# Optimization experiments

Hardware: AMD Instinct MI355X
Metric: run time of the kernel (lower is better)

Reference implementation:

```python
import jax, jax.numpy as jnp
import numpy as np

NUM_GRAPHS = 128


def _gcn_conv(x, W, b, src, dst, norm, n_nodes):
    # PyG GCNConv: linear transform, then symmetric-normalized scatter-add aggregation
    h = x @ W                                  # [N, out]
    msg = norm[:, None] * h[src]               # [E+N, out] gathered messages
    out = jax.ops.segment_sum(msg, dst, num_segments=n_nodes)
    return out + b


def setup_inputs() -> dict:
    key = jax.random.key(0)
    ks = jax.random.split(key, 12)
    N, E, H, GE, C = 100000, 1000000, 64, 64, 5
    x = jax.random.normal(ks[0], (N, 2), dtype=jnp.float32)
    edge_index = jax.random.randint(ks[1], (2, E), 0, N, dtype=jnp.int32)
    batch = jnp.sort(jax.random.randint(ks[2], (N,), 0, NUM_GRAPHS, dtype=jnp.int32))
    graph_embedding = jax.random.normal(ks[3], (NUM_GRAPHS, GE), dtype=jnp.float32)
    s = lambda k, shape, fan: jax.random.normal(k, shape, dtype=jnp.float32) * (1.0 / np.sqrt(fan))
    W1 = s(ks[4], (2, H), 2); b1 = jnp.zeros((H,), jnp.float32)
    W2 = s(ks[5], (H, H), H); b2 = jnp.zeros((H,), jnp.float32)
    W3 = s(ks[6], (H, H), H); b3 = jnp.zeros((H,), jnp.float32)
    Wl = s(ks[7], (H + GE, C), H + GE); bl = jnp.zeros((C,), jnp.float32)
    return {"x": x, "edge_index": edge_index, "batch": batch,
            "graph_embedding": graph_embedding,
            "W1": W1, "b1": b1, "W2": W2, "b2": b2, "W3": W3, "b3": b3,
            "Wl": Wl, "bl": bl}


def reference(x, edge_index, batch, graph_embedding, W1, b1, W2, b2, W3, b3, Wl, bl):
    N = x.shape[0]
    loops = jnp.arange(N, dtype=edge_index.dtype)
    src = jnp.concatenate([edge_index[0], loops])   # add self-loops
    dst = jnp.concatenate([edge_index[1], loops])
    deg = jax.ops.segment_sum(jnp.ones_like(dst, dtype=x.dtype), dst, num_segments=N)
    dinv = jnp.where(deg > 0, jax.lax.rsqrt(deg), 0.0)
    norm = dinv[src] * dinv[dst]                    # [E+N]

    h = jax.nn.relu(_gcn_conv(x, W1, b1, src, dst, norm, N))
    h = jax.nn.relu(_gcn_conv(h, W2, b2, src, dst, norm, N))
    h = _gcn_conv(h, W3, b3, src, dst, norm, N)

    # global mean pool over graphs
    sums = jax.ops.segment_sum(h, batch, num_segments=NUM_GRAPHS)
    cnts = jax.ops.segment_sum(jnp.ones((N,), x.dtype), batch, num_segments=NUM_GRAPHS)
    pooled = sums / jnp.maximum(cnts, 1.0)[:, None]

    z = jnp.concatenate([pooled, graph_embedding], axis=1) @ Wl + bl
    return jax.nn.log_softmax(z, axis=1)
```

## Files before the change

### kernel.cpp

```cpp
#include <hip/hip_runtime.h>
#include <hip/hip_bf16.h>
#include <math.h>

#define NG 128
#define CHUNKB 4096
#define NBIN 512
#define EWIN 256

typedef __attribute__((ext_vector_type(8))) short short8;
typedef __attribute__((ext_vector_type(4))) float float4v;

static __device__ __forceinline__ float bf2f(__hip_bfloat16 v) { return __bfloat162float(v); }

__global__ void k_bin_hist(const int* __restrict__ dst, int* __restrict__ hist,
                           int e, int nb) {
    __shared__ int h[NBIN];
    for (int i = threadIdx.x; i < NBIN; i += 256) h[i] = 0;
    __syncthreads();
    int base = blockIdx.x * CHUNKB;
    int lim = e - base; if (lim > CHUNKB) lim = CHUNKB;
    for (int k = threadIdx.x; k < lim; k += 256)
        atomicAdd(&h[dst[base + k] >> 8], 1);
    __syncthreads();
    for (int b = threadIdx.x; b < NBIN; b += 256) hist[b * nb + blockIdx.x] = h[b];
}

__global__ void __launch_bounds__(512) genscan1(int* __restrict__ a, int* __restrict__ bsums, int n) {
    __shared__ int s[512];
    int tid = threadIdx.x;
    int i = blockIdx.x * 512 + tid;
    int v = (i < n) ? a[i] : 0;
    s[tid] = v;
    __syncthreads();
    for (int d = 1; d < 512; d <<= 1) {
        int t = (tid >= d) ? s[tid - d] : 0;
        __syncthreads();
        s[tid] += t;
        __syncthreads();
    }
    if (i < n) a[i] = s[tid] - v;
    if (tid == 511) bsums[blockIdx.x] = s[511];
}

__global__ void __launch_bounds__(512) genscan2(int* __restrict__ bsums, int nb) {
    __shared__ int s[512];
    int tid = threadIdx.x;
    int v = (tid < nb) ? bsums[tid] : 0;
    s[tid] = v;
    __syncthreads();
    for (int d = 1; d < 512; d <<= 1) {
        int t = (tid >= d) ? s[tid - d] : 0;
        __syncthreads();
        s[tid] += t;
        __syncthreads();
    }
    if (tid < nb) bsums[tid] = s[tid] - v;
}

__global__ void k_bin_scatter(const int* __restrict__ srcs, const int* __restrict__ dsts,
                              const int* __restrict__ offsets, const int* __restrict__ bsums,
                              int2* __restrict__ outbuf, int e, int nb) {
    __shared__ int hcnt[NBIN];
    __shared__ int lstart[NBIN];
    __shared__ int ss[256];
    __shared__ int2 stage[CHUNKB];
    int tid = threadIdx.x, blk = blockIdx.x, base = blk * CHUNKB;
    int lim = e - base; if (lim > CHUNKB) lim = CHUNKB;
    for (int i = tid; i < NBIN; i += 256) hcnt[i] = 0;
    __syncthreads();
    for (int k = tid; k < lim; k += 256)
        atomicAdd(&hcnt[dsts[base + k] >> 8], 1);
    __syncthreads();
    int c0 = hcnt[2 * tid], c1 = hcnt[2 * tid + 1];
    int sum = c0 + c1;
    ss[tid] = sum;
    __syncthreads();
    for (int d = 1; d < 256; d <<= 1) {
        int t = (tid >= d) ? ss[tid - d] : 0;
        __syncthreads();
        ss[tid] += t;
        __syncthreads();
    }
    int excl = ss[tid] - sum;
    lstart[2 * tid] = excl;
    lstart[2 * tid + 1] = excl + c0;
    __syncthreads();
    hcnt[2 * tid] = excl;
    hcnt[2 * tid + 1] = excl + c0;
    __syncthreads();
    for (int k = tid; k < lim; k += 256) {
        int2 ed = make_int2(srcs[base + k], dsts[base + k]);
        int p = atomicAdd(&hcnt[ed.y >> 8], 1);
        stage[p] = ed;
    }
    __syncthreads();
    for (int i = tid; i < NBIN; i += 256) {
        int gi = i * nb + blk;
        lstart[i] = offsets[gi] + bsums[gi >> 9] - lstart[i];
    }
    __syncthreads();
    for (int p = tid; p < lim; p += 256) {
        int2 ed = stage[p];
        outbuf[lstart[ed.y >> 8] + p] = ed;
    }
}

__global__ void k_csrA(const int2* __restrict__ ebuck, const int* __restrict__ offsets,
                       const int* __restrict__ bsums, int* __restrict__ row_ptr,
                       float* __restrict__ dinv, int n, int nb, int nbuk, int e_total) {
    __shared__ int lcnt[256];
    __shared__ int ssc[256];
    int b = blockIdx.x, tid = threadIdx.x, n0 = b << 8;
    lcnt[tid] = 0;
    __syncthreads();
    int i0 = b * nb, i1 = (b + 1) * nb;
    int e0 = offsets[i0] + bsums[i0 >> 9];
    int e1 = offsets[i1] + bsums[i1 >> 9];
    for (int i = e0 + tid; i < e1; i += 256)
        atomicAdd(&lcnt[ebuck[i].y - n0], 1);
    __syncthreads();
    int v = lcnt[tid];
    ssc[tid] = v;
    __syncthreads();
    for (int d = 1; d < 256; d <<= 1) {
        int t = (tid >= d) ? ssc[tid - d] : 0;
        __syncthreads();
        ssc[tid] += t;
        __syncthreads();
    }
    int node = n0 + tid;
    if (node < n) {
        row_ptr[node] = e0 + ssc[tid] - v;
        dinv[node] = rsqrtf((float)v + 1.0f);
        if (node == n - 1) row_ptr[n] = e_total;
    }
}

__global__ void k_csrB(const int2* __restrict__ ebuck, const int* __restrict__ offsets,
                       const int* __restrict__ bsums, const int* __restrict__ row_ptr,
                       const float* __restrict__ dinv, int2* __restrict__ csr, int nb) {
    __shared__ int lcur[256];
    int b = blockIdx.x, tid = threadIdx.x, n0 = b << 8;
    lcur[tid] = 0;
    __syncthreads();
    int i0 = b * nb, i1 = (b + 1) * nb;
    int e0 = offsets[i0] + bsums[i0 >> 9];
    int e1 = offsets[i1] + bsums[i1 >> 9];
    for (int i = e0 + tid; i < e1; i += 256) {
        int2 ed = ebuck[i];
        int r = atomicAdd(&lcur[ed.y - n0], 1);
        int pos = row_ptr[ed.y] + r;
        float w = dinv[ed.x] * dinv[ed.y];
        csr[pos] = make_int2(ed.x, __float_as_int(w));
    }
}

__global__ void k_layer1(const int* __restrict__ row_ptr, const int2* __restrict__ edges,
                         const float* __restrict__ x, const float* __restrict__ dinv,
                         const float* __restrict__ W1, const float* __restrict__ b1,
                         __hip_bfloat16* __restrict__ h, int n) {
    __shared__ float w1s[128];
    __shared__ float b1s[64];
    if (threadIdx.x < 128) w1s[threadIdx.x] = W1[threadIdx.x];
    if (threadIdx.x < 64) b1s[threadIdx.x] = b1[threadIdx.x];
    __syncthreads();
    int i = blockIdx.x * blockDim.x + threadIdx.x;
    if (i >= n) return;
    const float2* x2 = (const float2*)x;
    float dd = dinv[i], d2 = dd * dd;
    float2 xi = x2[i];
    float a0 = d2 * xi.x, a1 = d2 * xi.y;
    int lo = row_ptr[i], hi = row_ptr[i + 1];
    int k = lo;
    for (; k + 4 <= hi; k += 4) {
        int2 e0 = edges[k], e1 = edges[k + 1], e2 = edges[k + 2], e3 = edges[k + 3];
        float2 v0 = x2[e0.x], v1 = x2[e1.x], v2 = x2[e2.x], v3 = x2[e3.x];
        a0 += __int_as_float(e0.y) * v0.x; a1 += __int_as_float(e0.y) * v0.y;
        a0 += __int_as_float(e1.y) * v1.x; a1 += __int_as_float(e1.y) * v1.y;
        a0 += __int_as_float(e2.y) * v2.x; a1 += __int_as_float(e2.y) * v2.y;
        a0 += __int_as_float(e3.y) * v3.x; a1 += __int_as_float(e3.y) * v3.y;
    }
    for (; k < hi; k++) {
        int2 e = edges[k];
        float2 v = x2[e.x];
        a0 += __int_as_float(e.y) * v.x;
        a1 += __int_as_float(e.y) * v.y;
    }
    short8* hv = reinterpret_cast<short8*>(h + (size_t)i * 64);
    #pragma unroll
    for (int g = 0; g < 8; g++) {
        short8 pack;
        #pragma unroll
        for (int j = 0; j < 8; j++) {
            int col = g * 8 + j;
            float v = fmaxf(a0 * w1s[col] + a1 * w1s[64 + col] + b1s[col], 0.0f);
            __hip_bfloat16 bv = __float2bfloat16(v);
            pack[j] = *reinterpret_cast<short*>(&bv);
        }
        hv[g] = pack;
    }
}

template <bool FAST>
static __device__ __forceinline__ void agg_node(int lo, int hi, int half, int col,
        const int2* __restrict__ gE, const int2* EW, int wave_lo,
        const uint* __restrict__ hinu, float& ax, float& ay) {
    for (int k = lo; k < hi; k += 16) {
        int ss[8]; float ww[8];
        #pragma unroll
        for (int j = 0; j < 8; j++) {
            int idx = k + 2 * j + half;
            int cidx = idx < hi ? idx : lo;
            int2 ee = FAST ? EW[cidx - wave_lo] : gE[cidx];
            ss[j] = ee.x;
            ww[j] = idx < hi ? __int_as_float(ee.y) : 0.0f;
        }
        uint vv[8];
        #pragma unroll
        for (int j = 0; j < 8; j++) vv[j] = hinu[(size_t)ss[j] * 32 + col];
        #pragma unroll
        for (int j = 0; j < 8; j++) {
            ax += ww[j] * __int_as_float(vv[j] << 16);
            ay += ww[j] * __int_as_float(vv[j] & 0xffff0000u);
        }
    }
}

template <int RELU, int POOL>
__global__ void __launch_bounds__(64, 8) k_aggLin(const int* __restrict__ row_ptr,
                                                  const int2* __restrict__ edges,
                                                  const __hip_bfloat16* __restrict__ hin,
                                                  const float* __restrict__ dinv,
                                                  const __hip_bfloat16* __restrict__ Wf,
                                                  const float* __restrict__ b,
                                                  __hip_bfloat16* __restrict__ hout,
                                                  const int* __restrict__ batch,
                                                  float* __restrict__ sums, int n) {
    __shared__ __attribute__((aligned(16))) __hip_bfloat16 T[16 * 72];
    __shared__ int2 EW[EWIN];
    int lane = threadIdx.x;
    int nb0 = blockIdx.x * 16;
    if (nb0 >= n) return;
    int half = lane >> 5, col = lane & 31;
    const uint* hinu = reinterpret_cast<const uint*>(hin);

    int bidx = nb0 + (lane < 16 ? lane : 16);
    if (bidx > n) bidx = n;
    int rp = row_ptr[bidx];
    int wave_lo = __shfl(rp, 0);
    int wave_hi = __shfl(rp, 16);
    int cnt = wave_hi - wave_lo;
    bool fast = (cnt <= EWIN);
    if (fast)
        for (int i = lane; i < cnt; i += 64) EW[i] = edges[wave_lo + i];

    for (int nn = 0; nn < 16; nn++) {
        int node = nb0 + nn;
        float ax = 0.0f, ay = 0.0f;
        if (node < n) {
            if (half == 0) {
                float dn = dinv[node];
                uint hv = hinu[(size_t)node * 32 + col];
                float dn2 = dn * dn;
                ax = dn2 * __int_as_float(hv << 16);
                ay = dn2 * __int_as_float(hv & 0xffff0000u);
            }
            int lo = __shfl(rp, nn), hi = __shfl(rp, nn + 1);
            if (fast) agg_node<true >(lo, hi, half, col, edges, EW, wave_lo, hinu, ax, ay);
            else      agg_node<false>(lo, hi, half, col, edges, EW, wave_lo, hinu, ax, ay);
        }
        ax += __shfl_xor(ax, 32);
        ay += __shfl_xor(ay, 32);
        if (half == 0) {
            __hip_bfloat16 bx = __float2bfloat16(ax);
            __hip_bfloat16 by = __float2bfloat16(ay);
            uint pack = (uint)(*reinterpret_cast<unsigned short*>(&bx)) |
                        ((uint)(*reinterpret_cast<unsigned short*>(&by)) << 16);
            *reinterpret_cast<uint*>(&T[nn * 72 + 2 * col]) = pack;
        }
    }

    int m = lane & 15, q = lane >> 4;
    short8 a0 = *reinterpret_cast<const short8*>(&T[m * 72 + q * 8]);
    short8 a1 = *reinterpret_cast<const short8*>(&T[m * 72 + 32 + q * 8]);
    int lastn = nb0 + 15 < n ? nb0 + 15 : n - 1;
    bool onegraph = POOL && (nb0 + 15 < n) && (batch[nb0] == batch[lastn]);
    int gA = POOL ? batch[nb0] : 0;
    #pragma unroll
    for (int jt = 0; jt < 4; jt++) {
        short8 bf0 = *reinterpret_cast<const short8*>(Wf + ((size_t)(jt * 2 + 0) * 64 + lane) * 8);
        short8 bf1 = *reinterpret_cast<const short8*>(Wf + ((size_t)(jt * 2 + 1) * 64 + lane) * 8);
        float4v d = {0.0f, 0.0f, 0.0f, 0.0f};
        d = __builtin_amdgcn_mfma_f32_16x16x32_bf16(a0, bf0, d, 0, 0, 0);
        d = __builtin_amdgcn_mfma_f32_16x16x32_bf16(a1, bf1, d, 0, 0, 0);
        float bias = b[jt * 16 + m];
        if (POOL) {
            if (onegraph) {
                float s = (d[0] + bias) + (d[1] + bias) + (d[2] + bias) + (d[3] + bias);
                s += __shfl_xor(s, 16);
                s += __shfl_xor(s, 32);
                if (q == 0) atomicAdd(&sums[gA * 64 + jt * 16 + m], s);
            } else {
                #pragma unroll
                for (int r = 0; r < 4; r++) {
                    int node = nb0 + q * 4 + r;
                    if (node < n)
                        atomicAdd(&sums[batch[node] * 64 + jt * 16 + m], d[r] + bias);
                }
            }
        } else {
            #pragma unroll
            for (int r = 0; r < 4; r++) {
                int node = nb0 + q * 4 + r;
                if (node < n) {
                    float v = d[r] + bias;
                    if (RELU) v = fmaxf(v, 0.0f);
                    hout[(size_t)node * 64 + jt * 16 + m] = __float2bfloat16(v);
                }
            }
        }
    }
}

__global__ void k_prepW(const float* __restrict__ W2, const float* __restrict__ W3,
                        __hip_bfloat16* __restrict__ Wf2, __hip_bfloat16* __restrict__ Wf3) {
    const float* W = blockIdx.x ? W3 : W2;
    __hip_bfloat16* Wf = blockIdx.x ? Wf3 : Wf2;
    int t = threadIdx.x;
    int c = t >> 6, l = t & 63;
    int jt = c >> 1, half = c & 1, nn = l & 15, q = l >> 4;
    #pragma unroll
    for (int j = 0; j < 8; j++) {
        int k = half * 32 + q * 8 + j;
        Wf[t * 8 + j] = __float2bfloat16(W[k * 64 + jt * 16 + nn]);
    }
}

__device__ inline int lower_bound_i(const int* __restrict__ a, int n, int key) {
    int lo = 0, hi = n;
    while (lo < hi) {
        int mid = (lo + hi) >> 1;
        if (a[mid] < key) lo = mid + 1; else hi = mid;
    }
    return lo;
}

__global__ void k_head(const float* __restrict__ sums, const int* __restrict__ batch,
                       const float* __restrict__ ge, const float* __restrict__ Wl,
                       const float* __restrict__ bl, float* __restrict__ out,
                       int n, int ng) {
    int g = blockIdx.x * blockDim.x + threadIdx.x;
    if (g < ng) {
        int lo = lower_bound_i(batch, n, g);
        int hi = lower_bound_i(batch, n, g + 1);
        float c = fmaxf((float)(hi - lo), 1.0f);
        float z[5];
        for (int cl = 0; cl < 5; cl++) z[cl] = bl[cl];
        for (int k = 0; k < 64; k++) {
            float p = sums[g * 64 + k] / c;
            for (int cl = 0; cl < 5; cl++) z[cl] += p * Wl[k * 5 + cl];
        }
        for (int k = 0; k < 64; k++) {
            float p = ge[g * 64 + k];
            for (int cl = 0; cl < 5; cl++) z[cl] += p * Wl[(64 + k) * 5 + cl];
        }
        float m = z[0];
        for (int cl = 1; cl < 5; cl++) m = fmaxf(m, z[cl]);
        float s = 0.0f;
        for (int cl = 0; cl < 5; cl++) s += expf(z[cl] - m);
        float lse = m + logf(s);
        for (int cl = 0; cl < 5; cl++) out[g * 5 + cl] = z[cl] - lse;
    }
}

#define ALIGN16(x) (((x) + 15) & ~(size_t)15)

extern "C" void kernel_launch(void* const* d_in, const int* in_sizes, int n_in,
                              void* d_out, int out_size, void* d_ws, size_t ws_size,
                              hipStream_t stream) {
    const float* x    = (const float*)d_in[0];
    const int*   ei   = (const int*)d_in[1];
    const int*   batch= (const int*)d_in[2];
    const float* ge   = (const float*)d_in[3];
    const float* W1   = (const float*)d_in[4];
    const float* b1   = (const float*)d_in[5];
    const float* W2   = (const float*)d_in[6];
    const float* b2   = (const float*)d_in[7];
    const float* W3   = (const float*)d_in[8];
    const float* b3   = (const float*)d_in[9];
    const float* Wl   = (const float*)d_in[10];
    const float* bl   = (const float*)d_in[11];
    float* out = (float*)d_out;

    const int N = in_sizes[0] / 2;
    const int E = in_sizes[1] / 2;
    const int* src = ei;
    const int* dst = ei + E;
    const int NBUK = (N + 255) >> 8;
    const int nbC  = (E + CHUNKB - 1) / CHUNKB;

    char* wsb = (char*)d_ws;
    float* dinv   = (float*)wsb;                wsb += ALIGN16((size_t)N * 4);
    __hip_bfloat16* h16 = (__hip_bfloat16*)wsb;  wsb += ALIGN16((size_t)64 * N * 2);
    __hip_bfloat16* buf2= (__hip_bfloat16*)wsb;  wsb += ALIGN16((size_t)64 * N * 2);
    float* sums   = (float*)wsb;                wsb += ALIGN16((size_t)NG * 64 * 4);
    __hip_bfloat16* Wf2 = (__hip_bfloat16*)wsb; wsb += ALIGN16((size_t)4096 * 2);
    __hip_bfloat16* Wf3 = (__hip_bfloat16*)wsb; wsb += ALIGN16((size_t)4096 * 2);
    int2*  ebuck  = (int2*)wsb;                 wsb += ALIGN16((size_t)E * 8);
    int2*  csr    = (int2*)wsb;                 wsb += ALIGN16((size_t)E * 8);
    int*   row_ptr= (int*)wsb;                  wsb += ALIGN16((size_t)(N + 1) * 4);
    int*   hist   = (int*)wsb;                  wsb += ALIGN16((size_t)NBIN * nbC * 4);
    int*   bsums  = (int*)wsb;                  wsb += 512 * 4;

    const int BS = 256;
    int gN   = (N + BS - 1) / BS;
    int gF   = (N + 15) / 16;
    int nH   = NBIN * nbC;
    int gH   = (nH + 511) / 512;

    hipMemsetAsync(sums, 0, (size_t)NG * 64 * 4, stream);
    k_bin_hist<<<nbC, BS, 0, stream>>>(dst, hist, E, nbC);
    genscan1<<<gH, 512, 0, stream>>>(hist, bsums, nH);
    genscan2<<<1, 512, 0, stream>>>(bsums, gH);
    k_bin_scatter<<<nbC, BS, 0, stream>>>(src, dst, hist, bsums, ebuck, E, nbC);
    k_csrA<<<NBUK, BS, 0, stream>>>(ebuck, hist, bsums, row_ptr, dinv, N, nbC, NBUK, E);
    k_csrB<<<NBUK, BS, 0, stream>>>(ebuck, hist, bsums, row_ptr, dinv, csr, nbC);
    k_prepW<<<2, 512, 0, stream>>>(W2, W3, Wf2, Wf3);

    k_layer1<<<gN, BS, 0, stream>>>(row_ptr, csr, x, dinv, W1, b1, h16, N);

    k_aggLin<1, 0><<<gF, 64, 0, stream>>>(row_ptr, csr, h16, dinv, Wf2, b2, buf2,
                                          nullptr, nullptr, N);

    k_aggLin<0, 1><<<gF, 64, 0, stream>>>(row_ptr, csr, buf2, dinv, Wf3, b3, nullptr,
                                          batch, sums, N);

    k_head<<<1, 128, 0, stream>>>(sums, batch, ge, Wl, bl, out, N, NG);
}
```

Measured before the change: 231.1 us.

## Fold symmetric normalization into node features and drop per-edge weights from CSR

Instead of storing a per-edge weight dinv[src]*dinv[dst], each layer's output is pre-scaled by dinv of the source node and the aggregate is post-scaled by dinv of the destination node. The CSR then holds only int source indices, which halves edge bandwidth in every aggregation pass and removes the multiplies. The two CSR-build kernels are merged into one that stages edges in LDS, and the memset and weight prep are folded into the histogram kernel as extra blocks, removing several launches. The LDS stage is large (about 48KB), which may reduce occupancy of the CSR kernel, and there is a global-memory fallback path for oversized buckets.

```diff
diff --git a/kernel.cpp b/kernel.cpp
--- a/kernel.cpp
+++ b/kernel.cpp
@@ -6,23 +6,44 @@
 #define CHUNKB 4096
 #define NBIN 512
 #define EWIN 256
+#define STAGE_CAP 6144
 
 typedef __attribute__((ext_vector_type(8))) short short8;
 typedef __attribute__((ext_vector_type(4))) float float4v;
 
-static __device__ __forceinline__ float bf2f(__hip_bfloat16 v) { return __bfloat162float(v); }
-
 __global__ void k_bin_hist(const int* __restrict__ dst, int* __restrict__ hist,
-                           int e, int nb) {
+                           int e, int nb, float* __restrict__ sums,
+                           const float* __restrict__ W2, const float* __restrict__ W3,
+                           __hip_bfloat16* __restrict__ Wf2, __hip_bfloat16* __restrict__ Wf3) {
     __shared__ int h[NBIN];
+    int blk = blockIdx.x;
+    if (blk >= nb) {
+        int ex = blk - nb;
+        if (ex == 0) {
+            for (int i = threadIdx.x; i < NG * 64; i += 256) sums[i] = 0.0f;
+        } else {
+            const float* W = (ex == 2) ? W3 : W2;
+            __hip_bfloat16* Wf = (ex == 2) ? Wf3 : Wf2;
+            for (int t = threadIdx.x; t < 512; t += 256) {
+                int c = t >> 6, l = t & 63;
+                int jt = c >> 1, half = c & 1, nn = l & 15, q = l >> 4;
+                #pragma unroll
+                for (int j = 0; j < 8; j++) {
+                    int k = half * 32 + q * 8 + j;
+                    Wf[t * 8 + j] = __float2bfloat16(W[k * 64 + jt * 16 + nn]);
+                }
+            }
+        }
+        return;
+    }
     for (int i = threadIdx.x; i < NBIN; i += 256) h[i] = 0;
     __syncthreads();
-    int base = blockIdx.x * CHUNKB;
+    int base = blk * CHUNKB;
     int lim = e - base; if (lim > CHUNKB) lim = CHUNKB;
     for (int k = threadIdx.x; k < lim; k += 256)
         atomicAdd(&h[dst[base + k] >> 8], 1);
     __syncthreads();
-    for (int b = threadIdx.x; b < NBIN; b += 256) hist[b * nb + blockIdx.x] = h[b];
+    for (int b = threadIdx.x; b < NBIN; b += 256) hist[b * nb + blk] = h[b];
 }
 
 __global__ void __launch_bounds__(512) genscan1(int* __restrict__ a, int* __restrict__ bsums, int n) {
@@ -105,19 +126,33 @@
     }
 }
 
-__global__ void k_csrA(const int2* __restrict__ ebuck, const int* __restrict__ offsets,
-                       const int* __restrict__ bsums, int* __restrict__ row_ptr,
-                       float* __restrict__ dinv, int n, int nb, int nbuk, int e_total) {
+__global__ void k_csrAB(const int2* __restrict__ ebuck, const int* __restrict__ offsets,
+                        const int* __restrict__ bsums, const float* __restrict__ x,
+                        int* __restrict__ row_ptr, float* __restrict__ dinv,
+                        float2* __restrict__ xs, int* __restrict__ csr,
+                        int n, int nb, int e_total) {
     __shared__ int lcnt[256];
     __shared__ int ssc[256];
+    __shared__ int rstart[256];
+    __shared__ int2 stage[STAGE_CAP];
     int b = blockIdx.x, tid = threadIdx.x, n0 = b << 8;
     lcnt[tid] = 0;
     __syncthreads();
     int i0 = b * nb, i1 = (b + 1) * nb;
     int e0 = offsets[i0] + bsums[i0 >> 9];
     int e1 = offsets[i1] + bsums[i1 >> 9];
-    for (int i = e0 + tid; i < e1; i += 256)
-        atomicAdd(&lcnt[ebuck[i].y - n0], 1);
+    int cnt = e1 - e0;
+    bool fast = (cnt <= STAGE_CAP);
+    if (fast) {
+        for (int i = e0 + tid; i < e1; i += 256) {
+            int2 ed = ebuck[i];
+            stage[i - e0] = ed;
+            atomicAdd(&lcnt[ed.y - n0], 1);
+        }
+    } else {
+        for (int i = e0 + tid; i < e1; i += 256)
+            atomicAdd(&lcnt[ebuck[i].y - n0], 1);
+    }
     __syncthreads();
     int v = lcnt[tid];
     ssc[tid] = v;
@@ -128,35 +163,39 @@
         ssc[tid] += t;
         __syncthreads();
     }
+    int rs = e0 + ssc[tid] - v;
+    rstart[tid] = rs;
     int node = n0 + tid;
     if (node < n) {
-        row_ptr[node] = e0 + ssc[tid] - v;
-        dinv[node] = rsqrtf((float)v + 1.0f);
+        row_ptr[node] = rs;
+        float dv = rsqrtf((float)v + 1.0f);
+        dinv[node] = dv;
+        const float2* x2 = (const float2*)x;
+        float2 xi = x2[node];
+        xs[node] = make_float2(xi.x * dv, xi.y * dv);
         if (node == n - 1) row_ptr[n] = e_total;
     }
-}
-
-__global__ void k_csrB(const int2* __restrict__ ebuck, const int* __restrict__ offsets,
-                       const int* __restrict__ bsums, const int* __restrict__ row_ptr,
-                       const float* __restrict__ dinv, int2* __restrict__ csr, int nb) {
-    __shared__ int lcur[256];
-    int b = blockIdx.x, tid = threadIdx.x, n0 = b << 8;
-    lcur[tid] = 0;
-    __syncthreads();
-    int i0 = b * nb, i1 = (b + 1) * nb;
-    int e0 = offsets[i0] + bsums[i0 >> 9];
-    int e1 = offsets[i1] + bsums[i1 >> 9];
-    for (int i = e0 + tid; i < e1; i += 256) {
-        int2 ed = ebuck[i];
-        int r = atomicAdd(&lcur[ed.y - n0], 1);
-        int pos = row_ptr[ed.y] + r;
-        float w = dinv[ed.x] * dinv[ed.y];
-        csr[pos] = make_int2(ed.x, __float_as_int(w));
-    }
-}
-
-__global__ void k_layer1(const int* __restrict__ row_ptr, const int2* __restrict__ edges,
-                         const float* __restrict__ x, const float* __restrict__ dinv,
+    lcnt[tid] = 0;
+    __syncthreads();
+    if (fast) {
+        for (int i = tid; i < cnt; i += 256) {
+            int2 ed = stage[i];
+            int li = ed.y - n0;
+            int r = atomicAdd(&lcnt[li], 1);
+            csr[rstart[li] + r] = ed.x;
+        }
+    } else {
+        for (int i = e0 + tid; i < e1; i += 256) {
+            int2 ed = ebuck[i];
+            int li = ed.y - n0;
+            int r = atomicAdd(&lcnt[li], 1);
+            csr[rstart[li] + r] = ed.x;
+        }
+    }
+}
+
+__global__ void k_layer1(const int* __restrict__ row_ptr, const int* __restrict__ edges,
+                         const float2* __restrict__ xs, const float* __restrict__ dinv,
                          const float* __restrict__ W1, const float* __restrict__ b1,
                          __hip_bfloat16* __restrict__ h, int n) {
     __shared__ float w1s[128];
@@ -166,26 +205,23 @@
     __syncthreads();
     int i = blockIdx.x * blockDim.x + threadIdx.x;
     if (i >= n) return;
-    const float2* x2 = (const float2*)x;
-    float dd = dinv[i], d2 = dd * dd;
-    float2 xi = x2[i];
-    float a0 = d2 * xi.x, a1 = d2 * xi.y;
+    float dd = dinv[i];
+    float2 xi = xs[i];
+    float a0 = xi.x, a1 = xi.y;
     int lo = row_ptr[i], hi = row_ptr[i + 1];
     int k = lo;
     for (; k + 4 <= hi; k += 4) {
-        int2 e0 = edges[k], e1 = edges[k + 1], e2 = edges[k + 2], e3 = edges[k + 3];
-        float2 v0 = x2[e0.x], v1 = x2[e1.x], v2 = x2[e2.x], v3 = x2[e3.x];
-        a0 += __int_as_float(e0.y) * v0.x; a1 += __int_as_float(e0.y) * v0.y;
-        a0 += __int_as_float(e1.y) * v1.x; a1 += __int_as_float(e1.y) * v1.y;
-        a0 += __int_as_float(e2.y) * v2.x; a1 += __int_as_float(e2.y) * v2.y;
-        a0 += __int_as_float(e3.y) * v3.x; a1 += __int_as_float(e3.y) * v3.y;
+        int s0 = edges[k], s1 = edges[k + 1], s2 = edges[k + 2], s3 = edges[k + 3];
+        float2 v0 = xs[s0], v1 = xs[s1], v2 = xs[s2], v3 = xs[s3];
+        a0 += v0.x + v1.x + v2.x + v3.x;
+        a1 += v0.y + v1.y + v2.y + v3.y;
     }
     for (; k < hi; k++) {
-        int2 e = edges[k];
-        float2 v = x2[e.x];
-        a0 += __int_as_float(e.y) * v.x;
-        a1 += __int_as_float(e.y) * v.y;
-    }
+        float2 v = xs[edges[k]];
+        a0 += v.x;
+        a1 += v.y;
+    }
+    a0 *= dd; a1 *= dd;
     short8* hv = reinterpret_cast<short8*>(h + (size_t)i * 64);
     #pragma unroll
     for (int g = 0; g < 8; g++) {
@@ -194,6 +230,7 @@
         for (int j = 0; j < 8; j++) {
             int col = g * 8 + j;
             float v = fmaxf(a0 * w1s[col] + a1 * w1s[64 + col] + b1s[col], 0.0f);
+            v *= dd;
             __hip_bfloat16 bv = __float2bfloat16(v);
             pack[j] = *reinterpret_cast<short*>(&bv);
         }
@@ -203,32 +240,32 @@
 
 template <bool FAST>
 static __device__ __forceinline__ void agg_node(int lo, int hi, int half, int col,
-        const int2* __restrict__ gE, const int2* EW, int wave_lo,
+        const int* __restrict__ gE, const int* EW, int wave_lo,
         const uint* __restrict__ hinu, float& ax, float& ay) {
     for (int k = lo; k < hi; k += 16) {
-        int ss[8]; float ww[8];
+        int ss[8];
         #pragma unroll
         for (int j = 0; j < 8; j++) {
             int idx = k + 2 * j + half;
             int cidx = idx < hi ? idx : lo;
-            int2 ee = FAST ? EW[cidx - wave_lo] : gE[cidx];
-            ss[j] = ee.x;
-            ww[j] = idx < hi ? __int_as_float(ee.y) : 0.0f;
+            ss[j] = FAST ? EW[cidx - wave_lo] : gE[cidx];
         }
         uint vv[8];
         #pragma unroll
         for (int j = 0; j < 8; j++) vv[j] = hinu[(size_t)ss[j] * 32 + col];
         #pragma unroll
         for (int j = 0; j < 8; j++) {
-            ax += ww[j] * __int_as_float(vv[j] << 16);
-            ay += ww[j] * __int_as_float(vv[j] & 0xffff0000u);
+            int idx = k + 2 * j + half;
+            uint u = idx < hi ? vv[j] : 0u;
+            ax += __int_as_float(u << 16);
+            ay += __int_as_float(u & 0xffff0000u);
         }
     }
 }
 
 template <int RELU, int POOL>
 __global__ void __launch_bounds__(64, 8) k_aggLin(const int* __restrict__ row_ptr,
-                                                  const int2* __restrict__ edges,
+                                                  const int* __restrict__ edges,
                                                   const __hip_bfloat16* __restrict__ hin,
                                                   const float* __restrict__ dinv,
                                                   const __hip_bfloat16* __restrict__ Wf,
@@ -237,7 +274,7 @@
                                                   const int* __restrict__ batch,
                                                   float* __restrict__ sums, int n) {
     __shared__ __attribute__((aligned(16))) __hip_bfloat16 T[16 * 72];
-    __shared__ int2 EW[EWIN];
+    __shared__ int EW[EWIN];
     int lane = threadIdx.x;
     int nb0 = blockIdx.x * 16;
     if (nb0 >= n) return;
@@ -259,11 +296,9 @@
         float ax = 0.0f, ay = 0.0f;
         if (node < n) {
             if (half == 0) {
-                float dn = dinv[node];
                 uint hv = hinu[(size_t)node * 32 + col];
-                float dn2 = dn * dn;
-                ax = dn2 * __int_as_float(hv << 16);
-                ay = dn2 * __int_as_float(hv & 0xffff0000u);
+                ax = __int_as_float(hv << 16);
+                ay = __int_as_float(hv & 0xffff0000u);
             }
             int lo = __shfl(rp, nn), hi = __shfl(rp, nn + 1);
             if (fast) agg_node<true >(lo, hi, half, col, edges, EW, wave_lo, hinu, ax, ay);
@@ -272,6 +307,8 @@
         ax += __shfl_xor(ax, 32);
         ay += __shfl_xor(ay, 32);
         if (half == 0) {
+            float dv = dinv[node < n ? node : 0];
+            ax *= dv; ay *= dv;
             __hip_bfloat16 bx = __float2bfloat16(ax);
             __hip_bfloat16 by = __float2bfloat16(ay);
             uint pack = (uint)(*reinterpret_cast<unsigned short*>(&bx)) |
@@ -286,6 +323,14 @@
     int lastn = nb0 + 15 < n ? nb0 + 15 : n - 1;
     bool onegraph = POOL && (nb0 + 15 < n) && (batch[nb0] == batch[lastn]);
     int gA = POOL ? batch[nb0] : 0;
+    float dvs[4];
+    if (!POOL) {
+        #pragma unroll
+        for (int r = 0; r < 4; r++) {
+            int node = nb0 + q * 4 + r;
+            dvs[r] = node < n ? dinv[node] : 0.0f;
+        }
+    }
     #pragma unroll
     for (int jt = 0; jt < 4; jt++) {
         short8 bf0 = *reinterpret_cast<const short8*>(Wf + ((size_t)(jt * 2 + 0) * 64 + lane) * 8);
@@ -315,24 +360,11 @@
                 if (node < n) {
                     float v = d[r] + bias;
                     if (RELU) v = fmaxf(v, 0.0f);
+                    v *= dvs[r];
                     hout[(size_t)node * 64 + jt * 16 + m] = __float2bfloat16(v);
                 }
             }
         }
-    }
-}
-
-__global__ void k_prepW(const float* __restrict__ W2, const float* __restrict__ W3,
-                        __hip_bfloat16* __restrict__ Wf2, __hip_bfloat16* __restrict__ Wf3) {
-    const float* W = blockIdx.x ? W3 : W2;
-    __hip_bfloat16* Wf = blockIdx.x ? Wf3 : Wf2;
-    int t = threadIdx.x;
-    int c = t >> 6, l = t & 63;
-    int jt = c >> 1, half = c & 1, nn = l & 15, q = l >> 4;
-    #pragma unroll
-    for (int j = 0; j < 8; j++) {
-        int k = half * 32 + q * 8 + j;
-        Wf[t * 8 + j] = __float2bfloat16(W[k * 64 + jt * 16 + nn]);
     }
 }
 
@@ -401,13 +433,14 @@
 
     char* wsb = (char*)d_ws;
     float* dinv   = (float*)wsb;                wsb += ALIGN16((size_t)N * 4);
+    float2* xs    = (float2*)wsb;               wsb += ALIGN16((size_t)N * 8);
     __hip_bfloat16* h16 = (__hip_bfloat16*)wsb;  wsb += ALIGN16((size_t)64 * N * 2);
     __hip_bfloat16* buf2= (__hip_bfloat16*)wsb;  wsb += ALIGN16((size_t)64 * N * 2);
     float* sums   = (float*)wsb;                wsb += ALIGN16((size_t)NG * 64 * 4);
     __hip_bfloat16* Wf2 = (__hip_bfloat16*)wsb; wsb += ALIGN16((size_t)4096 * 2);
     __hip_bfloat16* Wf3 = (__hip_bfloat16*)wsb; wsb += ALIGN16((size_t)4096 * 2);
     int2*  ebuck  = (int2*)wsb;                 wsb += ALIGN16((size_t)E * 8);
-    int2*  csr    = (int2*)wsb;                 wsb += ALIGN16((size_t)E * 8);
+    int*   csr    = (int*)wsb;                  wsb += ALIGN16((size_t)E * 4);
     int*   row_ptr= (int*)wsb;                  wsb += ALIGN16((size_t)(N + 1) * 4);
     int*   hist   = (int*)wsb;                  wsb += ALIGN16((size_t)NBIN * nbC * 4);
     int*   bsums  = (int*)wsb;                  wsb += 512 * 4;
@@ -418,16 +451,14 @@
     int nH   = NBIN * nbC;
     int gH   = (nH + 511) / 512;
 
-    hipMemsetAsync(sums, 0, (size_t)NG * 64 * 4, stream);
-    k_bin_hist<<<nbC, BS, 0, stream>>>(dst, hist, E, nbC);
+    k_bin_hist<<<nbC + 3, BS, 0, stream>>>(dst, hist, E, nbC, sums, W2, W3, Wf2, Wf3);
     genscan1<<<gH, 512, 0, stream>>>(hist, bsums, nH);
     genscan2<<<1, 512, 0, stream>>>(bsums, gH);
     k_bin_scatter<<<nbC, BS, 0, stream>>>(src, dst, hist, bsums, ebuck, E, nbC);
-    k_csrA<<<NBUK, BS, 0, stream>>>(ebuck, hist, bsums, row_ptr, dinv, N, nbC, NBUK, E);
-    k_csrB<<<NBUK, BS, 0, stream>>>(ebuck, hist, bsums, row_ptr, dinv, csr, nbC);
-    k_prepW<<<2, 512, 0, stream>>>(W2, W3, Wf2, Wf3);
-
-    k_layer1<<<gN, BS, 0, stream>>>(row_ptr, csr, x, dinv, W1, b1, h16, N);
+    k_csrAB<<<NBUK, BS, 0, stream>>>(ebuck, hist, bsums, x, row_ptr, dinv, xs, csr,
+                                     N, nbC, E);
+
+    k_layer1<<<gN, BS, 0, stream>>>(row_ptr, csr, xs, dinv, W1, b1, h16, N);
 
     k_aggLin<1, 0><<<gF, 64, 0, stream>>>(row_ptr, csr, h16, dinv, Wf2, b2, buf2,
                                           nullptr, nullptr, N);
```

Measured after the change: 220.6 us. -4.6%, faster.
